# Kernel optimization log

Hardware: AMD Instinct MI355X
Metric: run time of the kernel (lower is better)

Reference implementation:

```python
import jax, jax.numpy as jnp
import numpy as np

N = 262144        # BS(16) * MAX_FRAMES(256) * num_joints(64), flattened
D_IN = 4          # IN_FEAT: (x, y, z, conf) per joint
D_OUT = 512       # OUT_FEAT
NUM_JOINTS = 64   # embedding vocab size
PAD_FRAC = 0.1


def _uniform(key, shape, fan_in):
    s = 1.0 / np.sqrt(fan_in)
    return jax.random.uniform(key, shape, jnp.float32, minval=-s, maxval=s)


def setup_inputs() -> dict:
    key = jax.random.key(0)
    ks = jax.random.split(key, 12)
    joint_info = jax.random.normal(ks[0], (N, D_IN), jnp.float32)
    pad = jax.random.uniform(ks[1], (N,)) < PAD_FRAC
    joint_info = jnp.where(pad[:, None], 0.0, joint_info)  # all-zero rows = padding
    joint_token = jax.random.randint(ks[2], (N,), 0, NUM_JOINTS)
    emb = jax.random.normal(ks[3], (NUM_JOINTS, D_OUT), jnp.float32)
    W1 = _uniform(ks[4], (D_OUT // 4, D_IN), D_IN)
    b1 = _uniform(ks[5], (D_OUT // 4,), D_IN)
    W2 = _uniform(ks[6], (D_OUT // 2, D_OUT // 4), D_OUT // 4)
    b2 = _uniform(ks[7], (D_OUT // 2,), D_OUT // 4)
    W3 = _uniform(ks[8], (D_OUT // 4, D_OUT // 2), D_OUT // 2)
    b3 = _uniform(ks[9], (D_OUT // 4,), D_OUT // 2)
    W4 = _uniform(ks[10], (D_OUT, D_OUT // 4), D_OUT // 4)  # last layer: no bias
    return {"joint_info": joint_info, "joint_token": joint_token, "emb": emb,
            "W1": W1, "b1": b1, "W2": W2, "b2": b2, "W3": W3, "b3": b3, "W4": W4}


def _mlp(x, layers):
    # residual when in/out widths match; GELU (exact, like torch nn.GELU) except after last layer
    out = x
    n = len(layers)
    for i, (W, b) in enumerate(layers):
        y = out @ W.T
        if b is not None:
            y = y + b
        out = y + out if y.shape[-1] == out.shape[-1] else y
        if i != n - 1:
            out = jax.nn.gelu(out, approximate=False)
    return out


def reference(joint_info, joint_token, emb, W1, b1, W2, b2, W3, b3, W4):
    layers = [(W1, b1), (W2, b2), (W3, b3), (W4, None)]
    out = _mlp(joint_info, layers)                 # [N, D_OUT]
    out = out + emb[joint_token]                   # embedding add for non-pad path
    pad_mask = jnp.all(joint_info == 0, axis=-1)   # [N]
    # pad rows get embedding(0); non-pad rows get MLP output + token embedding
    return jnp.where(pad_mask[:, None], emb[0], out)
```

## Files before the change

### kernel.cpp

```cpp
#include <hip/hip_runtime.h>
#include <math.h>


typedef float  f32x4  __attribute__((ext_vector_type(4)));
typedef short  s16x8  __attribute__((ext_vector_type(8)));
typedef __bf16 bf16x8 __attribute__((ext_vector_type(8)));

__device__ __forceinline__ unsigned short f2bf(float x) {
  unsigned u = __builtin_bit_cast(unsigned, x);
  u = (u + 0x7FFFu + ((u >> 16) & 1u)) >> 16;
  return (unsigned short)u;
}
__device__ __forceinline__ float gelu_exact(float x) {
  return 0.5f * x * (1.0f + erff(x * 0.70710678118654752f));
}
__device__ __forceinline__ void lds_fence() {
  asm volatile("s_waitcnt lgkmcnt(0)" ::: "memory");
  __builtin_amdgcn_sched_barrier(0);
}

__global__ void embed_prep(const float* __restrict__ W2, const float* __restrict__ W3,
                           const float* __restrict__ W4, short* __restrict__ ws) {
  int tid = blockIdx.x * 256 + threadIdx.x;
  const float* W; int K; int base; int e;
  if (tid < 4096)      { W = W2; K = 128; base = 0;     e = tid; }
  else if (tid < 8192) { W = W3; K = 256; base = 32768; e = tid - 4096; }
  else                 { W = W4; K = 128; base = 65536; e = tid - 8192; }
  int lane = e & 63, f = e >> 6;
  int kt = K >> 5;
  int nn = f / kt, kk = f - nn * kt;
  int n  = nn * 16 + (lane & 15);
  int k0 = kk * 32 + (lane >> 4) * 8;
  const float* src = W + n * K + k0;
  s16x8 v;
#pragma unroll
  for (int j = 0; j < 8; j++) v[j] = (short)f2bf(src[j]);
  *reinterpret_cast<s16x8*>(ws + base + e * 8) = v;
}

__global__ __launch_bounds__(256, 4) void embed_main(
    const float* __restrict__ jinfo, const int* __restrict__ jtok,
    const float* __restrict__ emb,   const float* __restrict__ W1,
    const float* __restrict__ b1,    const float* __restrict__ b2,
    const float* __restrict__ b3,    const short* __restrict__ wsW,
    float* __restrict__ out) {
  __shared__ short lds_act[4][4096];
  const int lane = threadIdx.x & 63;
  const int wave = threadIdx.x >> 6;
  const int q = lane >> 4, c = lane & 15;
  const int rowBase = blockIdx.x * 128 + wave * 32;
  short* S = lds_act[wave];

  const float4* jp = reinterpret_cast<const float4*>(jinfo);

  float4 x0 = jp[rowBase + c];
  float4 x1 = jp[rowBase + 16 + c];
  s16x8 a2s[2][4];
#pragma unroll
  for (int kk = 0; kk < 4; kk++) {
#pragma unroll
    for (int j = 0; j < 8; j++) {
      int f = kk * 32 + q * 8 + j;
      float4 w = reinterpret_cast<const float4*>(W1)[f];
      float bb = b1[f];
      float h0 = fmaf(w.x, x0.x, fmaf(w.y, x0.y, fmaf(w.z, x0.z, fmaf(w.w, x0.w, bb))));
      float h1 = fmaf(w.x, x1.x, fmaf(w.y, x1.y, fmaf(w.z, x1.z, fmaf(w.w, x1.w, bb))));
      a2s[0][kk][j] = (short)f2bf(gelu_exact(h0));
      a2s[1][kk][j] = (short)f2bf(gelu_exact(h1));
    }
  }

  const s16x8* fr2 = reinterpret_cast<const s16x8*>(wsW);
  const s16x8* fr3 = reinterpret_cast<const s16x8*>(wsW + 32768);
  const s16x8* fr4 = reinterpret_cast<const s16x8*>(wsW + 65536);

  s16x8 a3s[2][8];
#pragma unroll
  for (int h = 0; h < 2; h++) {
#pragma unroll
    for (int nn = 0; nn < 8; nn++) {
      int nng = h * 8 + nn;
      f32x4 ac0 = {0.f, 0.f, 0.f, 0.f}, ac1 = {0.f, 0.f, 0.f, 0.f};
#pragma unroll
      for (int kk = 0; kk < 4; kk++) {
        bf16x8 bfr = __builtin_bit_cast(bf16x8, fr2[(nng * 4 + kk) * 64 + lane]);
        ac0 = __builtin_amdgcn_mfma_f32_16x16x32_bf16(__builtin_bit_cast(bf16x8, a2s[0][kk]), bfr, ac0, 0, 0, 0);
        ac1 = __builtin_amdgcn_mfma_f32_16x16x32_bf16(__builtin_bit_cast(bf16x8, a2s[1][kk]), bfr, ac1, 0, 0, 0);
      }
      int col = nn * 16 + c;
      float bias = b2[h * 128 + col];
#pragma unroll
      for (int t = 0; t < 2; t++) {
        f32x4 av = t ? ac1 : ac0;
#pragma unroll
        for (int r = 0; r < 4; r++) {
          int m = t * 16 + q * 4 + r;
          S[m * 128 + ((((col >> 3) ^ m) & 15) << 3) + (col & 7)] =
              (short)f2bf(gelu_exact(av[r] + bias));
        }
      }
    }
    lds_fence();
#pragma unroll
    for (int t = 0; t < 2; t++) {
#pragma unroll
      for (int kk = 0; kk < 4; kk++) {
        int m = t * 16 + c;
        int b = kk * 4 + q;
        a3s[t][h * 4 + kk] = *reinterpret_cast<const s16x8*>(&S[m * 128 + (((b ^ m) & 15) << 3)]);
      }
    }
    lds_fence();
  }

#pragma unroll
  for (int nn = 0; nn < 8; nn++) {
    f32x4 ac0 = {0.f, 0.f, 0.f, 0.f}, ac1 = {0.f, 0.f, 0.f, 0.f};
#pragma unroll
    for (int kk = 0; kk < 8; kk++) {
      bf16x8 bfr = __builtin_bit_cast(bf16x8, fr3[(nn * 8 + kk) * 64 + lane]);
      ac0 = __builtin_amdgcn_mfma_f32_16x16x32_bf16(__builtin_bit_cast(bf16x8, a3s[0][kk]), bfr, ac0, 0, 0, 0);
      ac1 = __builtin_amdgcn_mfma_f32_16x16x32_bf16(__builtin_bit_cast(bf16x8, a3s[1][kk]), bfr, ac1, 0, 0, 0);
    }
    int col = nn * 16 + c;
    float bias = b3[col];
#pragma unroll
    for (int t = 0; t < 2; t++) {
      f32x4 av = t ? ac1 : ac0;
#pragma unroll
      for (int r = 0; r < 4; r++) {
        int m = t * 16 + q * 4 + r;
        S[m * 128 + ((((col >> 3) ^ m) & 15) << 3) + (col & 7)] =
            (short)f2bf(gelu_exact(av[r] + bias));
      }
    }
  }
  lds_fence();

  s16x8 a4s[2][4];
#pragma unroll
  for (int t = 0; t < 2; t++) {
#pragma unroll
    for (int kk = 0; kk < 4; kk++) {
      int m = t * 16 + c;
      int b = kk * 4 + q;
      a4s[t][kk] = *reinterpret_cast<const s16x8*>(&S[m * 128 + (((b ^ m) & 15) << 3)]);
    }
  }

  int   offE[8];
  float mul[8];
#pragma unroll
  for (int i = 0; i < 8; i++) {
    int t = i >> 2, r = i & 3;
    int row = rowBase + t * 16 + q * 4 + r;
    float4 x = jp[row];
    bool pad = (x.x == 0.f) && (x.y == 0.f) && (x.z == 0.f) && (x.w == 0.f);
    int tok = jtok[row];
    offE[i] = (pad ? 0 : tok) * 512;
    mul[i]  = pad ? 0.f : 1.f;
  }

#pragma unroll
  for (int nn = 0; nn < 32; nn++) {
    f32x4 ac0 = {0.f, 0.f, 0.f, 0.f}, ac1 = {0.f, 0.f, 0.f, 0.f};
#pragma unroll
    for (int kk = 0; kk < 4; kk++) {
      bf16x8 bfr = __builtin_bit_cast(bf16x8, fr4[(nn * 4 + kk) * 64 + lane]);
      ac0 = __builtin_amdgcn_mfma_f32_16x16x32_bf16(__builtin_bit_cast(bf16x8, a4s[0][kk]), bfr, ac0, 0, 0, 0);
      ac1 = __builtin_amdgcn_mfma_f32_16x16x32_bf16(__builtin_bit_cast(bf16x8, a4s[1][kk]), bfr, ac1, 0, 0, 0);
    }
    int col = nn * 16 + c;
#pragma unroll
    for (int t = 0; t < 2; t++) {
      f32x4 av = t ? ac1 : ac0;
#pragma unroll
      for (int r = 0; r < 4; r++) {
        int i = t * 4 + r;
        int row = rowBase + t * 16 + q * 4 + r;
        out[row * 512 + col] = av[r] * mul[i] + emb[offE[i] + col];
      }
    }
  }
}

extern "C" void kernel_launch(void* const* d_in, const int* in_sizes, int n_in,
                              void* d_out, int out_size, void* d_ws, size_t ws_size,
                              hipStream_t stream) {
  const float* jinfo = (const float*)d_in[0];
  const int*   jtok  = (const int*)d_in[1];
  const float* emb   = (const float*)d_in[2];
  const float* W1    = (const float*)d_in[3];
  const float* b1    = (const float*)d_in[4];
  const float* W2    = (const float*)d_in[5];
  const float* b2    = (const float*)d_in[6];
  const float* W3    = (const float*)d_in[7];
  const float* b3    = (const float*)d_in[8];
  const float* W4    = (const float*)d_in[9];
  float* out = (float*)d_out;
  short* ws  = (short*)d_ws;

  int rows = in_sizes[0] / 4;
  embed_prep<<<64, 256, 0, stream>>>(W2, W3, W4, ws);
  embed_main<<<rows / 128, 256, 0, stream>>>(jinfo, jtok, emb, W1, b1, b2, b3, ws, out);
}
```

Baseline: 986.3 us.

## Process layers 1-3 one 16-row tile at a time to cut register pressure

Layers 1-3 previously ran on both 16-row M-tiles at once. They now loop over one tile at a time with an unroll-1 loop, and each tile's layer-3 output is kept in its own LDS half-buffer for the final layer, which still runs on both tiles together. The goal is fewer live VGPRs (a2/a3 fragments and accumulators are halved) to ease register pressure or spills under launch_bounds(256,4). The cost is that every W2/W3 B-fragment is loaded from global/L2 twice instead of once and shared by two MFMAs, and less MFMA work is in flight to hide latency.

Measured after the change: 1.920 ms. 94.7% more time.

```diff
diff --git a/kernel.cpp b/kernel.cpp
--- a/kernel.cpp
+++ b/kernel.cpp
@@ -49,102 +49,90 @@
   const int wave = threadIdx.x >> 6;
   const int q = lane >> 4, c = lane & 15;
   const int rowBase = blockIdx.x * 128 + wave * 32;
-  short* S = lds_act[wave];
+  short* B0 = lds_act[wave];
+  short* B1 = lds_act[wave] + 2048;
 
   const float4* jp = reinterpret_cast<const float4*>(jinfo);
-
-  float4 x0 = jp[rowBase + c];
-  float4 x1 = jp[rowBase + 16 + c];
-  s16x8 a2s[2][4];
-#pragma unroll
-  for (int kk = 0; kk < 4; kk++) {
-#pragma unroll
-    for (int j = 0; j < 8; j++) {
-      int f = kk * 32 + q * 8 + j;
-      float4 w = reinterpret_cast<const float4*>(W1)[f];
-      float bb = b1[f];
-      float h0 = fmaf(w.x, x0.x, fmaf(w.y, x0.y, fmaf(w.z, x0.z, fmaf(w.w, x0.w, bb))));
-      float h1 = fmaf(w.x, x1.x, fmaf(w.y, x1.y, fmaf(w.z, x1.z, fmaf(w.w, x1.w, bb))));
-      a2s[0][kk][j] = (short)f2bf(gelu_exact(h0));
-      a2s[1][kk][j] = (short)f2bf(gelu_exact(h1));
-    }
-  }
-
   const s16x8* fr2 = reinterpret_cast<const s16x8*>(wsW);
   const s16x8* fr3 = reinterpret_cast<const s16x8*>(wsW + 32768);
   const s16x8* fr4 = reinterpret_cast<const s16x8*>(wsW + 65536);
 
-  s16x8 a3s[2][8];
+#pragma unroll 1
+  for (int t = 0; t < 2; ++t) {
+    float4 x = jp[rowBase + t * 16 + c];
+    s16x8 a2[4];
 #pragma unroll
-  for (int h = 0; h < 2; h++) {
+    for (int kk = 0; kk < 4; kk++) {
+#pragma unroll
+      for (int j = 0; j < 8; j++) {
+        int f = kk * 32 + q * 8 + j;
+        float4 w = reinterpret_cast<const float4*>(W1)[f];
+        float h = fmaf(w.x, x.x, fmaf(w.y, x.y, fmaf(w.z, x.z, fmaf(w.w, x.w, b1[f]))));
+        a2[kk][j] = (short)f2bf(gelu_exact(h));
+      }
+    }
+
+    s16x8 a3[8];
+#pragma unroll
+    for (int h = 0; h < 2; h++) {
+#pragma unroll
+      for (int nn = 0; nn < 8; nn++) {
+        int nng = h * 8 + nn;
+        f32x4 ac = {0.f, 0.f, 0.f, 0.f};
+#pragma unroll
+        for (int kk = 0; kk < 4; kk++) {
+          bf16x8 bfr = __builtin_bit_cast(bf16x8, fr2[(nng * 4 + kk) * 64 + lane]);
+          ac = __builtin_amdgcn_mfma_f32_16x16x32_bf16(__builtin_bit_cast(bf16x8, a2[kk]), bfr, ac, 0, 0, 0);
+        }
+        int col = nn * 16 + c;
+        float bias = b2[h * 128 + col];
+#pragma unroll
+        for (int r = 0; r < 4; r++) {
+          int m = q * 4 + r;
+          B1[m * 128 + ((((col >> 3) ^ m) & 15) << 3) + (col & 7)] =
+              (short)f2bf(gelu_exact(ac[r] + bias));
+        }
+      }
+      lds_fence();
+#pragma unroll
+      for (int kk = 0; kk < 4; kk++) {
+        int m = c;
+        int b = kk * 4 + q;
+        a3[h * 4 + kk] = *reinterpret_cast<const s16x8*>(&B1[m * 128 + (((b ^ m) & 15) << 3)]);
+      }
+      lds_fence();
+    }
+
+    short* Ht = t ? B1 : B0;
 #pragma unroll
     for (int nn = 0; nn < 8; nn++) {
-      int nng = h * 8 + nn;
-      f32x4 ac0 = {0.f, 0.f, 0.f, 0.f}, ac1 = {0.f, 0.f, 0.f, 0.f};
+      f32x4 ac = {0.f, 0.f, 0.f, 0.f};
 #pragma unroll
-      for (int kk = 0; kk < 4; kk++) {
-        bf16x8 bfr = __builtin_bit_cast(bf16x8, fr2[(nng * 4 + kk) * 64 + lane]);
-        ac0 = __builtin_amdgcn_mfma_f32_16x16x32_bf16(__builtin_bit_cast(bf16x8, a2s[0][kk]), bfr, ac0, 0, 0, 0);
-        ac1 = __builtin_amdgcn_mfma_f32_16x16x32_bf16(__builtin_bit_cast(bf16x8, a2s[1][kk]), bfr, ac1, 0, 0, 0);
+      for (int kk = 0; kk < 8; kk++) {
+        bf16x8 bfr = __builtin_bit_cast(bf16x8, fr3[(nn * 8 + kk) * 64 + lane]);
+        ac = __builtin_amdgcn_mfma_f32_16x16x32_bf16(__builtin_bit_cast(bf16x8, a3[kk]), bfr, ac, 0, 0, 0);
       }
       int col = nn * 16 + c;
-      float bias = b2[h * 128 + col];
+      float bias = b3[col];
 #pragma unroll
-      for (int t = 0; t < 2; t++) {
-        f32x4 av = t ? ac1 : ac0;
-#pragma unroll
-        for (int r = 0; r < 4; r++) {
-          int m = t * 16 + q * 4 + r;
-          S[m * 128 + ((((col >> 3) ^ m) & 15) << 3) + (col & 7)] =
-              (short)f2bf(gelu_exact(av[r] + bias));
-        }
-      }
-    }
-    lds_fence();
-#pragma unroll
-    for (int t = 0; t < 2; t++) {
-#pragma unroll
-      for (int kk = 0; kk < 4; kk++) {
-        int m = t * 16 + c;
-        int b = kk * 4 + q;
-        a3s[t][h * 4 + kk] = *reinterpret_cast<const s16x8*>(&S[m * 128 + (((b ^ m) & 15) << 3)]);
+      for (int r = 0; r < 4; r++) {
+        int m = q * 4 + r;
+        Ht[m * 128 + ((((col >> 3) ^ m) & 15) << 3) + (col & 7)] =
+            (short)f2bf(gelu_exact(ac[r] + bias));
       }
     }
     lds_fence();
   }
 
-#pragma unroll
-  for (int nn = 0; nn < 8; nn++) {
-    f32x4 ac0 = {0.f, 0.f, 0.f, 0.f}, ac1 = {0.f, 0.f, 0.f, 0.f};
-#pragma unroll
-    for (int kk = 0; kk < 8; kk++) {
-      bf16x8 bfr = __builtin_bit_cast(bf16x8, fr3[(nn * 8 + kk) * 64 + lane]);
-      ac0 = __builtin_amdgcn_mfma_f32_16x16x32_bf16(__builtin_bit_cast(bf16x8, a3s[0][kk]), bfr, ac0, 0, 0, 0);
-      ac1 = __builtin_amdgcn_mfma_f32_16x16x32_bf16(__builtin_bit_cast(bf16x8, a3s[1][kk]), bfr, ac1, 0, 0, 0);
-    }
-    int col = nn * 16 + c;
-    float bias = b3[col];
-#pragma unroll
-    for (int t = 0; t < 2; t++) {
-      f32x4 av = t ? ac1 : ac0;
-#pragma unroll
-      for (int r = 0; r < 4; r++) {
-        int m = t * 16 + q * 4 + r;
-        S[m * 128 + ((((col >> 3) ^ m) & 15) << 3) + (col & 7)] =
-            (short)f2bf(gelu_exact(av[r] + bias));
-      }
-    }
-  }
-  lds_fence();
-
   s16x8 a4s[2][4];
 #pragma unroll
   for (int t = 0; t < 2; t++) {
+    const short* Ht = t ? B1 : B0;
 #pragma unroll
     for (int kk = 0; kk < 4; kk++) {
-      int m = t * 16 + c;
+      int m = c;
       int b = kk * 4 + q;
-      a4s[t][kk] = *reinterpret_cast<const s16x8*>(&S[m * 128 + (((b ^ m) & 15) << 3)]);
+      a4s[t][kk] = *reinterpret_cast<const s16x8*>(&Ht[m * 128 + (((b ^ m) & 15) << 3)]);
     }
   }
 
@@ -154,8 +142,8 @@
   for (int i = 0; i < 8; i++) {
     int t = i >> 2, r = i & 3;
     int row = rowBase + t * 16 + q * 4 + r;
-    float4 x = jp[row];
-    bool pad = (x.x == 0.f) && (x.y == 0.f) && (x.z == 0.f) && (x.w == 0.f);
+    float4 xx = jp[row];
+    bool pad = (xx.x == 0.f) && (xx.y == 0.f) && (xx.z == 0.f) && (xx.w == 0.f);
     int tok = jtok[row];
     offE[i] = (pad ? 0 : tok) * 512;
     mul[i]  = pad ? 0.f : 1.f;
```
